# Kernel optimization log

Measured on AMD Instinct MI355X. Metric: run time of the kernel, lower is better.

## Reference

```python
import jax, jax.numpy as jnp
import numpy as np

LEAK = 0.95
THRESHOLD = 1.0
RESCALE = 2.0


def _xavier_uniform(key, shape, gain=2.0):
    fan_out, fan_in = shape
    bound = gain * np.sqrt(6.0 / (fan_in + fan_out))
    return jax.random.uniform(key, shape, jnp.float32, -bound, bound)


def setup_inputs() -> dict:
    key = jax.random.key(0)
    k_inp, k_w1, k_w2 = jax.random.split(key, 3)
    inp = jax.random.normal(k_inp, (8192, 784), jnp.float32)
    w1 = _xavier_uniform(k_w1, (800, 784))   # fc1.weight
    w2 = _xavier_uniform(k_w2, (10, 800))    # fc2.weight
    return {"inp": inp, "w1": w1, "w2": w2, "num_steps": 25}


@jax.custom_vjp
def spike_fn(x):
    return (x > 0).astype(x.dtype)

def _spike_fwd(x):
    return spike_fn(x), x

def _spike_bwd(x, g):
    # grad = g * 0.3 * relu(1 - |x|)  (surrogate BP)
    return (g * 0.3 * jnp.maximum(1.0 - jnp.abs(x), 0.0),)

spike_fn.defvjp(_spike_fwd, _spike_bwd)


def poisson_gen(key, inp):
    r = jax.random.uniform(key, inp.shape, inp.dtype)
    temp = (r * RESCALE <= jnp.abs(inp)).astype(inp.dtype) * jnp.sign(inp)
    return 0.5 * (temp + 1.0)


def reference(inp, w1, w2, num_steps):
    batch = inp.shape[0]
    x = inp.reshape(batch, -1)
    keys = jax.random.split(jax.random.key(42), num_steps)

    def step(carry, key):
        mem1, mem2 = carry
        sp = poisson_gen(key, x)                    # [B, 784]
        mem1 = LEAK * mem1 + (1.0 - LEAK) * (sp @ w1.T)  # [B, 800]
        mem_thr = mem1 / THRESHOLD - 1.0
        out = spike_fn(mem_thr)
        rst = jnp.where(mem_thr > 0, THRESHOLD, 0.0)
        mem1 = mem1 - jax.lax.stop_gradient(rst)
        mem2 = mem2 + out @ w2.T                    # [B, 10]
        return (mem1, mem2), None

    init = (jnp.zeros((batch, 800), x.dtype), jnp.zeros((batch, 10), x.dtype))
    (_, mem2), _ = jax.lax.scan(step, init, keys)
    return mem2 / num_steps
```

## Files before the change

kernel.cpp:

```cpp
#include <hip/hip_runtime.h>
#include <cstdint>

__host__ __device__ inline uint32_t tf_rotl32(uint32_t x, uint32_t r) {
  return (x << r) | (x >> (32u - r));
}

__host__ __device__ inline void threefry2x32(uint32_t k0, uint32_t k1,
                                             uint32_t x0, uint32_t x1,
                                             uint32_t* o0, uint32_t* o1) {
  uint32_t ks0 = k0, ks1 = k1, ks2 = k0 ^ k1 ^ 0x1BD11BDAu;
  x0 += ks0; x1 += ks1;
#define TF_R(r) { x0 += x1; x1 = tf_rotl32(x1, r); x1 ^= x0; }
  TF_R(13) TF_R(15) TF_R(26) TF_R(6)
  x0 += ks1; x1 += ks2 + 1u;
  TF_R(17) TF_R(29) TF_R(16) TF_R(24)
  x0 += ks2; x1 += ks0 + 2u;
  TF_R(13) TF_R(15) TF_R(26) TF_R(6)
  x0 += ks0; x1 += ks1 + 3u;
  TF_R(17) TF_R(29) TF_R(16) TF_R(24)
  x0 += ks1; x1 += ks2 + 4u;
  TF_R(13) TF_R(15) TF_R(26) TF_R(6)
  x0 += ks2; x1 += ks0 + 5u;
#undef TF_R
  *o0 = x0; *o1 = x1;
}

#define BSZ   8192
#define KIN   784
#define HID   800
#define NOUT  10
#define NSTEP 25


__global__ __launch_bounds__(256) void enc_kernel(const float* __restrict__ inp,
                                                  uint8_t* __restrict__ enc,
                                                  uint32_t k0, uint32_t k1) {
  int j = blockIdx.x * blockDim.x + threadIdx.x;
  if (j >= BSZ * KIN) return;
  uint32_t o0, o1;
  threefry2x32(k0, k1, 0u, (uint32_t)j, &o0, &o1);
  uint32_t bits = o0 ^ o1;
  float r = __uint_as_float((bits >> 9) | 0x3f800000u) - 1.0f;
  float x = inp[j];
  bool cond = (2.0f * r <= fabsf(x));
  int s = (x > 0.0f) ? 1 : ((x < 0.0f) ? -1 : 0);
  enc[j] = (uint8_t)(1 + (cond ? s : 0));
}

__global__ __launch_bounds__(256) void transpose_kernel(const float* __restrict__ w1,
                                                        float* __restrict__ w1t) {
  int idx = blockIdx.x * blockDim.x + threadIdx.x;
  if (idx >= KIN * HID) return;
  int k = idx / HID, n = idx % HID;
  w1t[idx] = w1[(size_t)n * KIN + k];
}

#define BM 256
#define BN 32
#define BK 16
#define GSTRIDE 272
#define WSTRIDE (4 * GSTRIDE)
#define BUFSZ   (4 * WSTRIDE)

typedef uint32_t u32;

__device__ __forceinline__ float cvt_ub(u32 x, int i) {
  return (float)((x >> (8 * i)) & 0xffu);
}

__device__ __forceinline__ void gload4(const void* g, void* l) {
  __builtin_amdgcn_global_load_lds(
      (const __attribute__((address_space(1))) void*)g,
      (__attribute__((address_space(3))) void*)l, 4, 0, 0);
}

__global__ __launch_bounds__(256) void gemm_kernel(const uint8_t* __restrict__ enc,
                                                   const float* __restrict__ w1t,
                                                   float* __restrict__ gp) {
  __shared__ uint8_t As[2][BUFSZ];
  const int panel  = blockIdx.z;
  const int kstart = panel * 264;
  const bool htail = (panel != 2);
  const int m0 = blockIdx.x * BM;
  const int n0 = blockIdx.y * BN;
  const int t  = threadIdx.x;
  const int lane = t & 63;
  const int wv   = t >> 6;

  const uint8_t* a_src = enc + (size_t)(m0 + wv * 64 + (lane >> 2)) * KIN
                         + kstart + (lane & 3) * 4;

  const int r0  = wv * 64 + lane;
  const int ard = wv * WSTRIDE + (lane >> 4) * GSTRIDE + (lane & 15) * 16;

  float acc[32];
#pragma unroll
  for (int c = 0; c < 32; c++) acc[c] = 0.0f;

#define ISSUE(P, TILE)                                                    \
  {                                                                       \
    _Pragma("unroll")                                                     \
    for (int q = 0; q < 4; q++)                                           \
      gload4(a_src + (size_t)(TILE) * BK + (size_t)(16 * q) * KIN,        \
             &As[P][wv * WSTRIDE + q * GSTRIDE]);                         \
  }

  ISSUE(0, 0)

  int p = 0;
  for (int tile = 0; tile < 16; tile++) {
    if (tile < 15) { ISSUE(p ^ 1, tile + 1) }
    else if (htail) { ISSUE(p ^ 1, 16) }
    uint4 s0 = *(const uint4*)&As[p][ard];
    const u32 w[4] = {s0.x, s0.y, s0.z, s0.w};
    const float* tb = w1t + (size_t)(kstart + tile * BK) * HID + n0;
#pragma unroll
    for (int kk = 0; kk < 16; kk++) {
      float a0 = cvt_ub(w[kk >> 2], kk & 3);
      const float* brow = tb + (size_t)kk * HID;
#pragma unroll
      for (int c = 0; c < 32; c++)
        acc[c] = __builtin_fmaf(a0, brow[c], acc[c]);
    }
    p ^= 1;
  }
  if (htail) {
    uint4 s0 = *(const uint4*)&As[p][ard];
    const u32 w[2] = {s0.x, s0.y};
    const float* tb = w1t + (size_t)(kstart + 256) * HID + n0;
#pragma unroll
    for (int kk = 0; kk < 8; kk++) {
      float a0 = cvt_ub(w[kk >> 2], kk & 3);
      const float* brow = tb + (size_t)kk * HID;
#pragma unroll
      for (int c = 0; c < 32; c++)
        acc[c] = __builtin_fmaf(a0, brow[c], acc[c]);
    }
  }
#undef ISSUE

  const size_t GS = (size_t)BSZ * HID;
  float* o0 = gp + (size_t)panel * GS + (size_t)(m0 + r0) * HID + n0;
#pragma unroll
  for (int c = 0; c < 32; c += 4) {
    float4 v0 = {acc[c], acc[c + 1], acc[c + 2], acc[c + 3]};
    *(float4*)(o0 + c) = v0;
  }
}

__global__ __launch_bounds__(256) void update_kernel(const float* __restrict__ gp,
                                                     float* __restrict__ mem1,
                                                     const float* __restrict__ w2,
                                                     float* __restrict__ mem2) {
  __shared__ float w2s[NOUT * HID];
  for (int i = threadIdx.x; i < NOUT * HID; i += 256) w2s[i] = w2[i];
  __syncthreads();

  const int wave = threadIdx.x / 64;
  const int lane = threadIdx.x % 64;
  const int b = blockIdx.x * 4 + wave;

  const size_t GS = (size_t)BSZ * HID;
  const float* g0 = gp + (size_t)b * HID;
  const float* g1 = g0 + GS;
  const float* g2 = g1 + GS;
  float* mrow = mem1 + (size_t)b * HID;

  float acc[NOUT];
#pragma unroll
  for (int i = 0; i < NOUT; i++) acc[i] = 0.0f;

  for (int j = lane; j < HID; j += 64) {
    float gs = __fmul_rn(0.5f, __fadd_rn(__fadd_rn(g0[j], g1[j]), g2[j]));
    float m = __fadd_rn(__fmul_rn(0.95f, mrow[j]), __fmul_rn(0.05f, gs));
    bool spike = __fadd_rn(m, -1.0f) > 0.0f;
    mrow[j] = spike ? __fadd_rn(m, -1.0f) : m;
    if (spike) {
#pragma unroll
      for (int i = 0; i < NOUT; i++) acc[i] += w2s[i * HID + j];
    }
  }
#pragma unroll
  for (int i = 0; i < NOUT; i++) {
    float v = acc[i];
    for (int off = 32; off > 0; off >>= 1) v += __shfl_down(v, off);
    if (lane == 0) mem2[(size_t)b * NOUT + i] += v;
  }
}

__global__ __launch_bounds__(256) void finalize_kernel(const float* __restrict__ mem2,
                                                       const int* __restrict__ ns,
                                                       float* __restrict__ out) {
  int i = blockIdx.x * blockDim.x + threadIdx.x;
  if (i < BSZ * NOUT) out[i] = mem2[i] / (float)(*ns);
}

extern "C" void kernel_launch(void* const* d_in, const int* in_sizes, int n_in,
                              void* d_out, int out_size, void* d_ws, size_t ws_size,
                              hipStream_t stream) {
  const float* inp = (const float*)d_in[0];
  const float* w1  = (const float*)d_in[1];
  const float* w2  = (const float*)d_in[2];
  const int*   dns = (const int*)d_in[3];
  float* out = (float*)d_out;

  char* ws = (char*)d_ws;
  size_t off = 0;
  uint8_t* enc = (uint8_t*)(ws + off);  off += (size_t)BSZ * KIN;
  off = (off + 255) & ~(size_t)255;
  float* w1t  = (float*)(ws + off);     off += (size_t)KIN * HID * 4;
  float* gp   = (float*)(ws + off);     off += (size_t)3 * BSZ * HID * 4;
  float* mem1 = (float*)(ws + off);     off += (size_t)BSZ * HID * 4;
  float* mem2 = (float*)(ws + off);     off += (size_t)BSZ * NOUT * 4;

  (void)hipMemsetAsync(mem1, 0, (size_t)BSZ * HID * 4, stream);
  (void)hipMemsetAsync(mem2, 0, (size_t)BSZ * NOUT * 4, stream);

  transpose_kernel<<<(KIN * HID + 255) / 256, 256, 0, stream>>>(w1, w1t);

  uint32_t keys[NSTEP][2];
  for (int t = 0; t < NSTEP; t++)
    threefry2x32(0u, 42u, 0u, (uint32_t)t, &keys[t][0], &keys[t][1]);

  const int n_elem = BSZ * KIN;
  for (int t = 0; t < NSTEP; t++) {
    enc_kernel<<<(n_elem + 255) / 256, 256, 0, stream>>>(inp, enc, keys[t][0], keys[t][1]);
    gemm_kernel<<<dim3(BSZ / BM, HID / BN, 3), 256, 0, stream>>>(enc, w1t, gp);
    update_kernel<<<BSZ / 4, 256, 0, stream>>>(gp, mem1, w2, mem2);
  }
  finalize_kernel<<<(BSZ * NOUT + 255) / 256, 256, 0, stream>>>(mem2, dns, out);
}
```

Before: 4.559 ms.

## Load encoded rows directly into registers and halve GEMM column tile

The GEMM kernel no longer stages the uint8 spike tile through LDS with async global_load_lds. Each thread now reads its own row's 16 bytes directly into registers, with register double-buffering. The column tile BN shrinks from 32 to 16, which doubles the grid and halves the accumulators per thread. The aim is to remove LDS traffic and raise occupancy, at the cost of uncoalesced per-row global loads (one row per lane, stride KIN) and twice as many re-reads of the A data across column blocks.

Result: faster. 4.293 ms (-5.9%).

```diff
diff --git a/kernel.cpp b/kernel.cpp
--- a/kernel.cpp
+++ b/kernel.cpp
@@ -56,28 +56,18 @@
 }
 
 #define BM 256
-#define BN 32
+#define BN 16
 #define BK 16
-#define GSTRIDE 272
-#define WSTRIDE (4 * GSTRIDE)
-#define BUFSZ   (4 * WSTRIDE)
 
 typedef uint32_t u32;
 
 __device__ __forceinline__ float cvt_ub(u32 x, int i) {
   return (float)((x >> (8 * i)) & 0xffu);
-}
-
-__device__ __forceinline__ void gload4(const void* g, void* l) {
-  __builtin_amdgcn_global_load_lds(
-      (const __attribute__((address_space(1))) void*)g,
-      (__attribute__((address_space(3))) void*)l, 4, 0, 0);
 }
 
 __global__ __launch_bounds__(256) void gemm_kernel(const uint8_t* __restrict__ enc,
                                                    const float* __restrict__ w1t,
                                                    float* __restrict__ gp) {
-  __shared__ uint8_t As[2][BUFSZ];
   const int panel  = blockIdx.z;
   const int kstart = panel * 264;
   const bool htail = (panel != 2);
@@ -87,62 +77,50 @@
   const int lane = t & 63;
   const int wv   = t >> 6;
 
-  const uint8_t* a_src = enc + (size_t)(m0 + wv * 64 + (lane >> 2)) * KIN
-                         + kstart + (lane & 3) * 4;
-
-  const int r0  = wv * 64 + lane;
-  const int ard = wv * WSTRIDE + (lane >> 4) * GSTRIDE + (lane & 15) * 16;
-
-  float acc[32];
-#pragma unroll
-  for (int c = 0; c < 32; c++) acc[c] = 0.0f;
-
-#define ISSUE(P, TILE)                                                    \
-  {                                                                       \
-    _Pragma("unroll")                                                     \
-    for (int q = 0; q < 4; q++)                                           \
-      gload4(a_src + (size_t)(TILE) * BK + (size_t)(16 * q) * KIN,        \
-             &As[P][wv * WSTRIDE + q * GSTRIDE]);                         \
-  }
-
-  ISSUE(0, 0)
-
-  int p = 0;
+  const int r0 = wv * 64 + lane;
+  const uint8_t* arow = enc + (size_t)(m0 + r0) * KIN + kstart;
+
+  float acc[16];
+#pragma unroll
+  for (int c = 0; c < 16; c++) acc[c] = 0.0f;
+
+  const int nld = htail ? 17 : 16;
+
+  uint4 acur = *(const uint4*)(arow);
+  uint4 anext;
+
   for (int tile = 0; tile < 16; tile++) {
-    if (tile < 15) { ISSUE(p ^ 1, tile + 1) }
-    else if (htail) { ISSUE(p ^ 1, 16) }
-    uint4 s0 = *(const uint4*)&As[p][ard];
-    const u32 w[4] = {s0.x, s0.y, s0.z, s0.w};
+    if (tile + 1 < nld)
+      anext = *(const uint4*)(arow + (size_t)(tile + 1) * BK);
+    const u32 w[4] = {acur.x, acur.y, acur.z, acur.w};
     const float* tb = w1t + (size_t)(kstart + tile * BK) * HID + n0;
 #pragma unroll
     for (int kk = 0; kk < 16; kk++) {
       float a0 = cvt_ub(w[kk >> 2], kk & 3);
       const float* brow = tb + (size_t)kk * HID;
 #pragma unroll
-      for (int c = 0; c < 32; c++)
+      for (int c = 0; c < 16; c++)
         acc[c] = __builtin_fmaf(a0, brow[c], acc[c]);
     }
-    p ^= 1;
+    acur = anext;
   }
   if (htail) {
-    uint4 s0 = *(const uint4*)&As[p][ard];
-    const u32 w[2] = {s0.x, s0.y};
+    const u32 w[2] = {acur.x, acur.y};
     const float* tb = w1t + (size_t)(kstart + 256) * HID + n0;
 #pragma unroll
     for (int kk = 0; kk < 8; kk++) {
       float a0 = cvt_ub(w[kk >> 2], kk & 3);
       const float* brow = tb + (size_t)kk * HID;
 #pragma unroll
-      for (int c = 0; c < 32; c++)
+      for (int c = 0; c < 16; c++)
         acc[c] = __builtin_fmaf(a0, brow[c], acc[c]);
     }
   }
-#undef ISSUE
 
   const size_t GS = (size_t)BSZ * HID;
   float* o0 = gp + (size_t)panel * GS + (size_t)(m0 + r0) * HID + n0;
 #pragma unroll
-  for (int c = 0; c < 32; c += 4) {
+  for (int c = 0; c < 16; c += 4) {
     float4 v0 = {acc[c], acc[c + 1], acc[c + 2], acc[c + 3]};
     *(float4*)(o0 + c) = v0;
   }
```
